# Optimization experiments

Hardware: AMD Instinct MI355X
Metric: run time of the kernel (lower is better)

## Reference

```python
import jax, jax.numpy as jnp
import numpy as np

T, B, DIM, N = 2, 256, 512, 196


def setup_inputs() -> dict:
    key = jax.random.key(0)
    ks = jax.random.split(key, 6)
    scale_mem = (2.0 / (DIM + DIM)) ** 0.5      # GlorotNormal
    scale_cat = (2.0 / (2 * DIM + DIM)) ** 0.5
    scale_attn = (2.0 / (DIM + 1)) ** 0.5
    return {
        "memory": jax.random.normal(ks[0], (T, B, DIM), dtype=jnp.float32),
        "know": jax.random.normal(ks[1], (B, DIM, N), dtype=jnp.float32),
        "control": jax.random.normal(ks[2], (T, B, DIM), dtype=jnp.float32),
        "W_mem": jax.random.normal(ks[3], (DIM, DIM), dtype=jnp.float32) * scale_mem,
        "b_mem": jnp.zeros((DIM,), dtype=jnp.float32),
        "W_concat": jax.random.normal(ks[4], (2 * DIM, DIM), dtype=jnp.float32) * scale_cat,
        "b_concat": jnp.zeros((DIM,), dtype=jnp.float32),
        "W_attn": jax.random.normal(ks[5], (DIM, 1), dtype=jnp.float32) * scale_attn,
        "b_attn": jnp.zeros((1,), dtype=jnp.float32),
    }


def reference(memory, know, control, W_mem, b_mem, W_concat, b_concat, W_attn, b_attn):
    # mem = Dense(dim)(memory[-1]) -> [B, dim]
    mem = memory[-1] @ W_mem + b_mem
    # mem[..., None] * know -> [B, dim, N]; concat along channel axis -> [B, 2*dim, N]
    cat = jnp.concatenate([mem[:, :, None] * know, know], axis=1)
    # transpose to [B, N, 2*dim], Dense(dim) -> [B, N, dim]
    concat = jnp.swapaxes(cat, 1, 2) @ W_concat + b_concat
    # gate by control[-1] -> [B, N, dim]; Dense(1) + squeeze -> [B, N]
    attn = concat * control[-1][:, None, :]
    logits = jnp.squeeze(attn @ W_attn, -1) + b_attn[0]
    # softmax over N, then (faithfully) weighted sum over the dim axis -> [B, N]
    a = jax.nn.softmax(logits, axis=1)[:, None, :]  # [B, 1, N]
    read = jnp.sum(a * know, axis=1)  # [B, N]
    return read
```

## Files before the change

kernel.cpp:

```cpp
#include <hip/hip_runtime.h>
#include <cfloat>

#define BB   256
#define DIM  512
#define NN   196

typedef __attribute__((ext_vector_type(8))) short bf16x8;
typedef __attribute__((ext_vector_type(4))) float f32x4;

__device__ __forceinline__ ushort f2bf(float x) {
    unsigned u = __float_as_uint(x);
    return (ushort)((u + 0x7FFFu + ((u >> 16) & 1u)) >> 16);
}

__global__ __launch_bounds__(256) void convert_kernel(
    const float* __restrict__ memory, const float* __restrict__ control,
    const float* __restrict__ W_mem, const float* __restrict__ W_concat,
    const float* __restrict__ W_attn,
    ushort* __restrict__ Wt,
    ushort* __restrict__ mu)
{
    const int tid = threadIdx.x;
    const int blk = blockIdx.x;

    if (blk < 512) {
        const int idx = blk * 256 + tid;
        const float4 q = ((const float4*)W_concat)[idx];
        uint2 o;
        o.x = (unsigned)f2bf(q.x) | ((unsigned)f2bf(q.y) << 16);
        o.y = (unsigned)f2bf(q.z) | ((unsigned)f2bf(q.w) << 16);
        ((uint2*)(Wt + (size_t)DIM * DIM))[idx] = o;
    } else if (blk < 576) {
        __shared__ float T[64][65];
        const int t  = blk - 512;
        const int tk = (t >> 3) * 64, ti = (t & 7) * 64;
        const int r  = tid >> 2;
        const int cb = (tid & 3) * 16;
        #pragma unroll
        for (int j = 0; j < 16; j += 4) {
            const float4 q = *(const float4*)&W_mem[(size_t)(tk + r) * DIM + ti + cb + j];
            T[r][cb + j + 0] = q.x; T[r][cb + j + 1] = q.y;
            T[r][cb + j + 2] = q.z; T[r][cb + j + 3] = q.w;
        }
        __syncthreads();
        const int ii = tid & 63;
        const int kq = tid >> 6;
        #pragma unroll
        for (int kk = 0; kk < 16; kk += 2) {
            const int k = kq * 16 + kk;
            const unsigned v = (unsigned)f2bf(T[k][ii]) | ((unsigned)f2bf(T[k + 1][ii]) << 16);
            *(unsigned*)&Wt[(size_t)(ti + ii) * DIM + tk + k] = v;
        }
    } else {
        const int idx = (blk - 576) * 256 + tid;
        const int sec = idx >> 15;
        const int j   = idx & 32767;
        const float4* src = sec ? (const float4*)(control + (size_t)BB * DIM)
                                : (const float4*)(memory  + (size_t)BB * DIM);
        float4 q = src[j];
        if (sec) {
            const float4 wa = ((const float4*)W_attn)[j & 127];
            q.x *= wa.x; q.y *= wa.y; q.z *= wa.z; q.w *= wa.w;
        }
        uint2 o;
        o.x = (unsigned)f2bf(q.x) | ((unsigned)f2bf(q.y) << 16);
        o.y = (unsigned)f2bf(q.z) | ((unsigned)f2bf(q.w) << 16);
        ((uint2*)mu)[(size_t)sec * 32768 + j] = o;
    }
}

__global__ __launch_bounds__(128) void prep_mfma(
    const ushort* __restrict__ Wt,
    const ushort* __restrict__ mu,
    const float* __restrict__ b_mem,
    float* __restrict__ w_out)
{
    __shared__ __align__(16) ushort mus[2][16][520];

    const int tid = threadIdx.x;
    const int wv  = tid >> 6;
    const int l   = tid & 63;
    const int b0  = blockIdx.x * 16;
    const int i0  = blockIdx.y * 32;

    #pragma unroll
    for (int p = 0; p < 16; ++p) {
        const int idx = p * 128 + tid;
        const int a   = idx >> 10;
        const int rb  = (idx >> 6) & 15;
        const int kc  = (idx & 63) * 8;
        *(uint4*)&mus[a][rb][kc] =
            *(const uint4*)&mu[((size_t)a * BB + b0 + rb) * DIM + kc];
    }
    __syncthreads();

    const int fr = l & 15;
    const int fk = (l >> 4) * 8;

    f32x4 accM = {0.f, 0.f, 0.f, 0.f};
    f32x4 acc1 = {0.f, 0.f, 0.f, 0.f};
    f32x4 acc2 = {0.f, 0.f, 0.f, 0.f};

    const int ib = i0 + wv * 16 + fr;
    const ushort* wm = Wt + ((size_t)0 * DIM + ib) * DIM;
    const ushort* c1 = Wt + ((size_t)1 * DIM + ib) * DIM;
    const ushort* c2 = Wt + ((size_t)2 * DIM + ib) * DIM;

    #pragma unroll 4
    for (int t = 0; t < 16; ++t) {
        const int k = t * 32 + fk;
        const bf16x8 am = *(const bf16x8*)&mus[0][fr][k];
        const bf16x8 au = *(const bf16x8*)&mus[1][fr][k];
        const bf16x8 bm = *(const bf16x8*)&wm[k];
        const bf16x8 b1 = *(const bf16x8*)&c1[k];
        const bf16x8 b2 = *(const bf16x8*)&c2[k];
        accM = __builtin_amdgcn_mfma_f32_16x16x32_bf16(am, bm, accM, 0, 0, 0);
        acc1 = __builtin_amdgcn_mfma_f32_16x16x32_bf16(au, b1, acc1, 0, 0, 0);
        acc2 = __builtin_amdgcn_mfma_f32_16x16x32_bf16(au, b2, acc2, 0, 0, 0);
    }

    const float bmv = b_mem[ib];
    const int rb0 = (l >> 4) * 4;
    #pragma unroll
    for (int r = 0; r < 4; ++r) {
        w_out[(size_t)(b0 + rb0 + r) * DIM + ib] =
            (accM[r] + bmv) * acc1[r] + acc2[r];
    }
}

__global__ __launch_bounds__(512, 4) void prep_fallback(
    const float* __restrict__ memory, const float* __restrict__ control,
    const float* __restrict__ W_mem, const float* __restrict__ b_mem,
    const float* __restrict__ W_concat, const float* __restrict__ W_attn,
    float* __restrict__ w_out)
{
    __shared__ float4 MU4[4][DIM];
    __shared__ float  buf[12288];

    const int tid = threadIdx.x;
    const int il  = tid & 31;
    const int kg  = tid >> 5;
    const int b0  = blockIdx.x * 8;
    const int i0  = blockIdx.y * 32;

    const float* mem_in = memory  + (size_t)BB * DIM;
    const float* ctl_in = control + (size_t)BB * DIM;

    {
        const float wa = W_attn[tid];
        #pragma unroll
        for (int p = 0; p < 4; ++p) {
            MU4[p][tid] = make_float4(
                mem_in[(size_t)(b0 + 2 * p)     * DIM + tid],
                ctl_in[(size_t)(b0 + 2 * p)     * DIM + tid] * wa,
                mem_in[(size_t)(b0 + 2 * p + 1) * DIM + tid],
                ctl_in[(size_t)(b0 + 2 * p + 1) * DIM + tid] * wa);
        }
    }

    float am[8] = {}, a1[8] = {}, a2[8] = {};
    const int sr = tid >> 4;
    const int sc = tid & 15;
    float2* WT = (float2*)buf;

    float4 f1 = *(const float4*)&W_concat[(size_t)(i0 + sr) * DIM + sc * 4];
    float4 f2 = *(const float4*)&W_concat[(size_t)(DIM + i0 + sr) * DIM + sc * 4];
    float wmc[4], wmn[4];
    #pragma unroll
    for (int j = 0; j < 4; ++j)
        wmc[j] = W_mem[(size_t)(kg * 4 + j) * DIM + i0 + il];

    for (int kt = 0; kt < DIM; kt += 64) {
        __syncthreads();
        {
            const float* f1f = (const float*)&f1;
            const float* f2f = (const float*)&f2;
            #pragma unroll
            for (int j = 0; j < 4; ++j)
                WT[(sc * 4 + j) * 33 + sr] = make_float2(f1f[j], f2f[j]);
        }
        if (kt + 64 < DIM) {
            f1 = *(const float4*)&W_concat[(size_t)(i0 + sr) * DIM + kt + 64 + sc * 4];
            f2 = *(const float4*)&W_concat[(size_t)(DIM + i0 + sr) * DIM + kt + 64 + sc * 4];
        }
        __syncthreads();
        if (kt + 64 < DIM) {
            #pragma unroll
            for (int j = 0; j < 4; ++j)
                wmn[j] = W_mem[(size_t)(kt + 64 + kg * 4 + j) * DIM + i0 + il];
        }
        #pragma unroll
        for (int j = 0; j < 4; ++j) {
            const int kl = kg * 4 + j;
            const int k  = kt + kl;
            const float2 c = WT[kl * 33 + il];
            #pragma unroll
            for (int p = 0; p < 4; ++p) {
                const float4 muv = MU4[p][k];
                am[2*p]   = fmaf(muv.x, wmc[j], am[2*p]);
                a1[2*p]   = fmaf(muv.y, c.x,    a1[2*p]);
                a2[2*p]   = fmaf(muv.y, c.y,    a2[2*p]);
                am[2*p+1] = fmaf(muv.z, wmc[j], am[2*p+1]);
                a1[2*p+1] = fmaf(muv.w, c.x,    a1[2*p+1]);
                a2[2*p+1] = fmaf(muv.w, c.y,    a2[2*p+1]);
            }
        }
        #pragma unroll
        for (int j = 0; j < 4; ++j) wmc[j] = wmn[j];
    }

    __syncthreads();
    #pragma unroll
    for (int b = 0; b < 8; ++b) {
        const int row = (kg * 8 + b) * 32 + il;
        buf[row]        = am[b];
        buf[4096 + row] = a1[b];
        buf[8192 + row] = a2[b];
    }
    __syncthreads();
    if (tid < 256) {
        const int rb = tid >> 5, ri = tid & 31;
        float sm = 0.f, s1 = 0.f, s2 = 0.f;
        #pragma unroll
        for (int t = 0; t < 16; ++t) {
            const int row = (t * 8 + rb) * 32 + ri;
            sm += buf[row];
            s1 += buf[4096 + row];
            s2 += buf[8192 + row];
        }
        w_out[(size_t)(b0 + rb) * DIM + i0 + ri] =
            (sm + b_mem[i0 + ri]) * s1 + s2;
    }
}

__global__ __launch_bounds__(1024) void read_kernel(
    const float* __restrict__ know,
    const float* __restrict__ w,
    float* __restrict__ out)
{
    __shared__ float  w_s[DIM];
    __shared__ float4 part_lg[16][50];
    __shared__ float4 part_ks[16][50];
    __shared__ float  tmp[256];
    __shared__ float  bc[2];

    const int tx  = threadIdx.x;
    const int ty  = threadIdx.y;
    const int tid = ty * 64 + tx;
    const int b   = blockIdx.x;

    if (tid < DIM) w_s[tid] = w[(size_t)b * DIM + tid];
    __syncthreads();

    float4 lg = make_float4(0.f, 0.f, 0.f, 0.f);
    float4 ks = make_float4(0.f, 0.f, 0.f, 0.f);
    if (tx < 49) {
        const float4* kp = (const float4*)(know + (size_t)b * DIM * NN) + (size_t)(ty * 32) * 49 + tx;
        const float*  wp = w_s + ty * 32;
        #pragma unroll 8
        for (int dd = 0; dd < 32; ++dd) {
            const float4 kv = kp[(size_t)dd * 49];
            const float  wv = wp[dd];
            lg.x = fmaf(kv.x, wv, lg.x); lg.y = fmaf(kv.y, wv, lg.y);
            lg.z = fmaf(kv.z, wv, lg.z); lg.w = fmaf(kv.w, wv, lg.w);
            ks.x += kv.x; ks.y += kv.y; ks.z += kv.z; ks.w += kv.w;
        }
        part_lg[ty][tx] = lg;
        part_ks[ty][tx] = ks;
    }
    __syncthreads();

    float lgn = 0.f, ksn = 0.f;
    if (tid < NN) {
        const int ng = tid >> 2, j = tid & 3;
        #pragma unroll
        for (int t = 0; t < 16; ++t) {
            lgn += ((const float*)&part_lg[t][ng])[j];
            ksn += ((const float*)&part_ks[t][ng])[j];
        }
    }

    if (tid < 256) tmp[tid] = (tid < NN) ? lgn : -FLT_MAX;
    __syncthreads();
    if (tid < 64) {
        float m = fmaxf(fmaxf(tmp[tid], tmp[tid + 64]),
                        fmaxf(tmp[tid + 128], tmp[tid + 192]));
        #pragma unroll
        for (int o = 32; o; o >>= 1) m = fmaxf(m, __shfl_down(m, o));
        if (tid == 0) bc[0] = m;
    }
    __syncthreads();

    const float e = (tid < NN) ? __expf(lgn - bc[0]) : 0.f;
    if (tid < 256) tmp[tid] = e;
    __syncthreads();
    if (tid < 64) {
        float s = tmp[tid] + tmp[tid + 64] + tmp[tid + 128] + tmp[tid + 192];
        #pragma unroll
        for (int o = 32; o; o >>= 1) s += __shfl_down(s, o);
        if (tid == 0) bc[1] = s;
    }
    __syncthreads();

    if (tid < NN) out[(size_t)b * NN + tid] = e / bc[1] * ksn;
}

extern "C" void kernel_launch(void* const* d_in, const int* in_sizes, int n_in,
                              void* d_out, int out_size, void* d_ws, size_t ws_size,
                              hipStream_t stream) {
    const float* memory   = (const float*)d_in[0];
    const float* know     = (const float*)d_in[1];
    const float* control  = (const float*)d_in[2];
    const float* W_mem    = (const float*)d_in[3];
    const float* b_mem    = (const float*)d_in[4];
    const float* W_concat = (const float*)d_in[5];
    const float* W_attn   = (const float*)d_in[7];
    float* outp = (float*)d_out;

    const size_t W_BYTES  = (size_t)BB * DIM * sizeof(float);
    const size_t WT_BYTES = (size_t)3 * DIM * DIM * sizeof(ushort);
    const size_t MU_BYTES = (size_t)2 * BB * DIM * sizeof(ushort);

    float* w_ws = (float*)d_ws;

    if (ws_size >= W_BYTES + WT_BYTES + MU_BYTES) {
        ushort* Wt = (ushort*)((char*)d_ws + W_BYTES);
        ushort* mu = (ushort*)((char*)d_ws + W_BYTES + WT_BYTES);
        convert_kernel<<<dim3(832), dim3(256), 0, stream>>>(
            memory, control, W_mem, W_concat, W_attn, Wt, mu);
        prep_mfma<<<dim3(BB / 16, DIM / 32), dim3(128), 0, stream>>>(
            Wt, mu, b_mem, w_ws);
    } else {
        prep_fallback<<<dim3(BB / 8, DIM / 32), dim3(512), 0, stream>>>(
            memory, control, W_mem, b_mem, W_concat, W_attn, w_ws);
    }
    read_kernel<<<dim3(BB), dim3(64, 16), 0, stream>>>(know, w_ws, outp);
}
```

Measured before the change: 32.87 us.

## Stage know tiles through shared memory with register prefetch in read kernel

The read kernel now loads the per-batch know slab in 64-row chunks using all 1024 threads with fully coalesced float4 loads. Each chunk goes into a 50KB shared buffer while the next chunk is prefetched into registers. Before this, only 49 of every 64 lanes issued strided global loads. The aim is better memory coalescing and overlap of loads with FMA work. In exchange it adds two barriers per chunk and a large shared-memory allocation that may limit occupancy.

```diff
diff --git a/kernel.cpp b/kernel.cpp
--- a/kernel.cpp
+++ b/kernel.cpp
@@ -238,6 +238,7 @@
     const float* __restrict__ w,
     float* __restrict__ out)
 {
+    __shared__ float4 buf4[3136];
     __shared__ float  w_s[DIM];
     __shared__ float4 part_lg[16][50];
     __shared__ float4 part_ks[16][50];
@@ -250,21 +251,48 @@
     const int b   = blockIdx.x;
 
     if (tid < DIM) w_s[tid] = w[(size_t)b * DIM + tid];
-    __syncthreads();
+
+    const float4* kb = (const float4*)(know + (size_t)b * DIM * NN);
+
+    float4 r0 = kb[tid];
+    float4 r1 = kb[1024 + tid];
+    float4 r2 = kb[2048 + tid];
+    float4 r3;
+    if (tid < 64) r3 = kb[3072 + tid];
 
     float4 lg = make_float4(0.f, 0.f, 0.f, 0.f);
     float4 ks = make_float4(0.f, 0.f, 0.f, 0.f);
+
+    for (int t = 0; t < 8; ++t) {
+        buf4[tid]        = r0;
+        buf4[1024 + tid] = r1;
+        buf4[2048 + tid] = r2;
+        if (tid < 64) buf4[3072 + tid] = r3;
+        __syncthreads();
+
+        if (t < 7) {
+            const float4* kn = kb + (t + 1) * 3136;
+            r0 = kn[tid];
+            r1 = kn[1024 + tid];
+            r2 = kn[2048 + tid];
+            if (tid < 64) r3 = kn[3072 + tid];
+        }
+
+        if (tx < 49) {
+            #pragma unroll
+            for (int rr = 0; rr < 4; ++rr) {
+                const int dl = ty * 4 + rr;
+                const float4 kv = buf4[dl * 49 + tx];
+                const float  wv = w_s[t * 64 + dl];
+                lg.x = fmaf(kv.x, wv, lg.x); lg.y = fmaf(kv.y, wv, lg.y);
+                lg.z = fmaf(kv.z, wv, lg.z); lg.w = fmaf(kv.w, wv, lg.w);
+                ks.x += kv.x; ks.y += kv.y; ks.z += kv.z; ks.w += kv.w;
+            }
+        }
+        __syncthreads();
+    }
+
     if (tx < 49) {
-        const float4* kp = (const float4*)(know + (size_t)b * DIM * NN) + (size_t)(ty * 32) * 49 + tx;
-        const float*  wp = w_s + ty * 32;
-        #pragma unroll 8
-        for (int dd = 0; dd < 32; ++dd) {
-            const float4 kv = kp[(size_t)dd * 49];
-            const float  wv = wp[dd];
-            lg.x = fmaf(kv.x, wv, lg.x); lg.y = fmaf(kv.y, wv, lg.y);
-            lg.z = fmaf(kv.z, wv, lg.z); lg.w = fmaf(kv.w, wv, lg.w);
-            ks.x += kv.x; ks.y += kv.y; ks.z += kv.z; ks.w += kv.w;
-        }
         part_lg[ty][tx] = lg;
         part_ks[ty][tx] = ks;
     }
```

Result: no change. 33.23 us (+1.1%).
